# Optimization experiments

Hardware: AMD Instinct MI355X
Metric: run time of the kernel (lower is better)

The kernel has to match this reference:

```python
import jax, jax.numpy as jnp
import numpy as np

N_NODES = 10000
N_EDGES = 320000
IN_DIM = 256
HID = 64
HEADS = 4
OUT_DIM = 64
NEG_SLOPE = 0.2


def setup_inputs() -> dict:
    key = jax.random.key(0)
    ks = jax.random.split(key, 10)
    s = 0.05
    return {
        "h": jax.random.normal(ks[0], (N_NODES, IN_DIM), jnp.float32),
        "src": jax.random.randint(ks[1], (N_EDGES,), 0, N_NODES, jnp.int32),
        "dst": jax.random.randint(ks[2], (N_EDGES,), 0, N_NODES, jnp.int32),
        "W1": jax.random.normal(ks[3], (IN_DIM, HEADS * HID), jnp.float32) * s,
        "al1": jax.random.normal(ks[4], (HEADS, HID), jnp.float32) * s,
        "ar1": jax.random.normal(ks[5], (HEADS, HID), jnp.float32) * s,
        "b1": jnp.zeros((HEADS * HID,), jnp.float32),
        "W2": jax.random.normal(ks[6], (HEADS * HID, OUT_DIM), jnp.float32) * s,
        "al2": jax.random.normal(ks[7], (1, OUT_DIM), jnp.float32) * s,
        "ar2": jax.random.normal(ks[8], (1, OUT_DIM), jnp.float32) * s,
        "b2": jnp.zeros((OUT_DIM,), jnp.float32),
    }


def _gatconv(h, W, al, ar, b, src, dst, n_heads, d_out):
    """DGL-style GATConv: project, edge-softmax attention, scatter-aggregate."""
    n = h.shape[0]
    feat = (h @ W).reshape(n, n_heads, d_out)          # [N,H,D]
    el = jnp.sum(feat * al, axis=-1)                   # [N,H]
    er = jnp.sum(feat * ar, axis=-1)                   # [N,H]
    e = jax.nn.leaky_relu(el[src] + er[dst], NEG_SLOPE)  # [E,H]
    # segment softmax over incoming edges of each dst node
    m = jax.ops.segment_max(e, dst, num_segments=n)    # [N,H]
    ex = jnp.exp(e - m[dst])                           # [E,H]
    denom = jax.ops.segment_sum(ex, dst, num_segments=n)  # [N,H]
    alpha = ex / denom[dst]                            # [E,H]
    msg = feat[src] * alpha[:, :, None]                # [E,H,D]
    out = jax.ops.segment_sum(msg, dst, num_segments=n)  # [N,H,D]
    return out + b.reshape(n_heads, d_out)


def reference(h, src, dst, W1, al1, ar1, b1, W2, al2, ar2, b2):
    h1 = _gatconv(h, W1, al1, ar1, b1, src, dst, HEADS, HID)
    h1 = jax.nn.elu(h1.reshape(N_NODES, HEADS * HID))  # flatten(1) then ELU
    h2 = _gatconv(h1, W2, al2, ar2, b2, src, dst, 1, OUT_DIM)
    return jnp.squeeze(h2, axis=1)  # [N, OUT_DIM]
```

## Files before the change

kernel.cpp:

```cpp
#include <hip/hip_runtime.h>
#include <hip/hip_bf16.h>
#include <stdint.h>

#define NN 10000
#define NE 320000
#define NH 4
#define BCAP 128

#define GEMM1_MB 79
#define GEMM1_BLOCKS (GEMM1_MB * 4)
#define BUILD_BLOCKS 1250

typedef __attribute__((ext_vector_type(8))) short s16x8;
typedef __attribute__((ext_vector_type(4))) float f32x4;
typedef __attribute__((ext_vector_type(8))) unsigned short u16x8;

static __device__ __forceinline__ float b2f(unsigned short u) {
    union { unsigned int i; float f; } x; x.i = ((unsigned int)u) << 16; return x.f;
}
static __device__ __forceinline__ unsigned short f2b(float f) {
    unsigned int u = __float_as_uint(f);
    unsigned int r = (u + 0x7fffu + ((u >> 16) & 1u)) >> 16;
    return (unsigned short)r;
}

__global__ __launch_bounds__(256) void k_prep(const unsigned short* __restrict__ hraw,
                        const void* __restrict__ W1, const void* __restrict__ W2,
                        const void* al1, const void* ar1, const void* b1,
                        const void* al2, const void* ar2, const void* b2,
                        unsigned short* __restrict__ W1T, unsigned short* __restrict__ W2T,
                        unsigned short* __restrict__ canon, int* __restrict__ cnt,
                        int* __restrict__ flag) {
    __shared__ int sb[256];
    int t = threadIdx.x;
    int c = 0;
    for (int i = t; i < 2048; i += 256) {
        unsigned short u = hraw[i];
        int e = (u >> 7) & 0xFF;
        c += (e >= 97 && e <= 157) ? 1 : 0;
    }
    sb[t] = c;
    __syncthreads();
    for (int o = 128; o > 0; o >>= 1) {
        if (t < o) sb[t] += sb[t + o];
        __syncthreads();
    }
    int isbf = (sb[0] >= 1741) ? 1 : 0;

    int idx = blockIdx.x * 256 + t;
    if (idx < 65536) {
        int n = idx >> 8, k = idx & 255;
        W1T[idx] = isbf ? ((const unsigned short*)W1)[k * 256 + n]
                        : f2b(((const float*)W1)[k * 256 + n]);
    } else if (idx < 81920) {
        int j = idx - 65536;
        int n = j >> 8, k = j & 255;
        W2T[j] = isbf ? ((const unsigned short*)W2)[k * 64 + n]
                      : f2b(((const float*)W2)[k * 64 + n]);
    } else if (idx < 82880) {
        int j = idx - 81920;
        const void* srcp; int q;
        if      (j < 256) { srcp = al1; q = j; }
        else if (j < 512) { srcp = ar1; q = j - 256; }
        else if (j < 768) { srcp = b1;  q = j - 512; }
        else if (j < 832) { srcp = al2; q = j - 768; }
        else if (j < 896) { srcp = ar2; q = j - 832; }
        else              { srcp = b2;  q = j - 896; }
        canon[j] = isbf ? ((const unsigned short*)srcp)[q] : f2b(((const float*)srcp)[q]);
    } else if (idx < 92880) {
        cnt[idx - 82880] = 0;
    } else if (idx == 92880) {
        flag[0] = isbf;
    }
}

#define BSTRIDE 264
static __device__ __forceinline__ void gemm_body(short* Bs,
                        const void* __restrict__ A, const unsigned short* __restrict__ BT,
                        unsigned short* __restrict__ C,
                        float* __restrict__ el, float* __restrict__ er,
                        const unsigned short* __restrict__ al,
                        const unsigned short* __restrict__ ar,
                        int M, int N, int H, int a_isbf, int mtile, int head) {
    int t = threadIdx.x;
    int wave = t >> 6, lane = t & 63;
    int m0 = mtile * 128;
    const unsigned short* Bh = BT + (size_t)head * 64 * 256;

#pragma unroll
    for (int i = 0; i < 8; ++i) {
        int idx = t + i * 256;
        int row = idx >> 5, chunk = idx & 31;
        *(s16x8*)&Bs[row * BSTRIDE + chunk * 8] =
            *(const s16x8*)&Bh[(size_t)row * 256 + chunk * 8];
    }
    __syncthreads();

    int kq = (lane >> 4) * 8;
    const unsigned short* Ab = (const unsigned short*)A;
    const float*          Af = (const float*)A;
    int aR[2];
#pragma unroll
    for (int mi = 0; mi < 2; ++mi) {
        int aRow = m0 + mi * 64 + wave * 16 + (lane & 15);
        aR[mi] = (aRow < M) ? aRow : M - 1;
    }
    f32x4 acc[2][4] = {};

#pragma unroll
    for (int k0 = 0; k0 < 256; k0 += 32) {
        s16x8 afr[2];
#pragma unroll
        for (int mi = 0; mi < 2; ++mi) {
            if (a_isbf) {
                afr[mi] = *(const s16x8*)&Ab[(size_t)aR[mi] * 256 + k0 + kq];
            } else {
                const float* pf = &Af[(size_t)aR[mi] * 256 + k0 + kq];
                float4 x0 = *(const float4*)pf;
                float4 x1 = *(const float4*)(pf + 4);
                afr[mi][0] = (short)f2b(x0.x); afr[mi][1] = (short)f2b(x0.y);
                afr[mi][2] = (short)f2b(x0.z); afr[mi][3] = (short)f2b(x0.w);
                afr[mi][4] = (short)f2b(x1.x); afr[mi][5] = (short)f2b(x1.y);
                afr[mi][6] = (short)f2b(x1.z); afr[mi][7] = (short)f2b(x1.w);
            }
        }
#pragma unroll
        for (int nt = 0; nt < 4; ++nt) {
            s16x8 bfr = *(const s16x8*)&Bs[(nt * 16 + (lane & 15)) * BSTRIDE + k0 + kq];
            acc[0][nt] = __builtin_amdgcn_mfma_f32_16x16x32_bf16(afr[0], bfr, acc[0][nt], 0, 0, 0);
            acc[1][nt] = __builtin_amdgcn_mfma_f32_16x16x32_bf16(afr[1], bfr, acc[1][nt], 0, 0, 0);
        }
    }

    float alv[4], arv[4];
#pragma unroll
    for (int nt = 0; nt < 4; ++nt) {
        int c = (lane & 15) + nt * 16;
        alv[nt] = b2f(al[head * 64 + c]);
        arv[nt] = b2f(ar[head * 64 + c]);
    }
    int col0 = head * 64 + (lane & 15);
#pragma unroll
    for (int mi = 0; mi < 2; ++mi) {
        int r0 = m0 + mi * 64 + wave * 16 + (lane >> 4) * 4;
        float cr[4][4];
#pragma unroll
        for (int nt = 0; nt < 4; ++nt) {
            int col = col0 + nt * 16;
#pragma unroll
            for (int i = 0; i < 4; ++i) {
                unsigned short cb = f2b(acc[mi][nt][i]);
                cr[nt][i] = b2f(cb);
                int r = r0 + i;
                if (r < M) C[(size_t)r * N + col] = cb;
            }
        }
#pragma unroll
        for (int i = 0; i < 4; ++i) {
            float pl = 0.f, pr = 0.f;
#pragma unroll
            for (int nt = 0; nt < 4; ++nt) {
                pl += cr[nt][i] * alv[nt];
                pr += cr[nt][i] * arv[nt];
            }
#pragma unroll
            for (int o = 1; o < 16; o <<= 1) {
                pl += __shfl_xor(pl, o, 64);
                pr += __shfl_xor(pr, o, 64);
            }
            int r = r0 + i;
            if ((lane & 15) == 0 && r < M) {
                el[(size_t)r * H + head] = pl;
                er[(size_t)r * H + head] = pr;
            }
        }
    }
}

__global__ __launch_bounds__(256) void k_g1b(const void* __restrict__ A,
                        const unsigned short* __restrict__ W1T,
                        unsigned short* __restrict__ feat1,
                        float* __restrict__ el, float* __restrict__ er,
                        const unsigned short* __restrict__ al,
                        const unsigned short* __restrict__ ar,
                        const int* __restrict__ flagp,
                        const int* __restrict__ src, const int* __restrict__ dst,
                        int* __restrict__ cnt, int* __restrict__ bucket) {
    __shared__ short Bs[64 * BSTRIDE];
    int bid = blockIdx.x;
    if (bid < GEMM1_BLOCKS) {
        int head = bid / GEMM1_MB;
        int mtile = bid - head * GEMM1_MB;
        gemm_body(Bs, A, W1T, feat1, el, er, al, ar, NN, 256, NH, flagp[0], mtile, head);
    } else {
        int i = (bid - GEMM1_BLOCKS) * 256 + threadIdx.x;
        if (i < NE) {
            int d = dst[i];
            int pos = atomicAdd(&cnt[d], 1);
            if (pos < BCAP) bucket[(d << 7) + pos] = src[i];
        }
    }
}

__global__ __launch_bounds__(256) void k_gemm(const void* __restrict__ A,
                                              const unsigned short* __restrict__ BT,
                                              unsigned short* __restrict__ C,
                                              float* __restrict__ el, float* __restrict__ er,
                                              const unsigned short* __restrict__ al,
                                              const unsigned short* __restrict__ ar,
                                              int M, int N, int H) {
    __shared__ short Bs[64 * BSTRIDE];
    gemm_body(Bs, A, BT, C, el, er, al, ar, M, N, H, 1, blockIdx.x, blockIdx.y);
}

__global__ __launch_bounds__(256) void k_edge1(const int* __restrict__ cnt,
                        const int* __restrict__ bucket,
                        const float* __restrict__ el, const float* __restrict__ er,
                        const unsigned short* __restrict__ feat,
                        const unsigned short* __restrict__ b1,
                        unsigned short* __restrict__ h1) {
    int wave = threadIdx.x >> 6, lane = threadIdx.x & 63;
    int node = blockIdx.x * 4 + wave;
    if (node >= NN) return;
    int eg = lane >> 3, d8 = lane & 7;
    int end = cnt[node]; if (end > BCAP) end = BCAP;
    const int* bkt = bucket + ((size_t)node << 7);
    float4 er4 = *(const float4*)&er[(size_t)node * 4];

    if (end <= 64) {
        int s = 0;
        float w0 = 0.f, w1 = 0.f, w2 = 0.f, w3 = 0.f;
        if (lane < end) {
            s = bkt[lane];
            float4 el4 = *(const float4*)&el[(size_t)s * 4];
            float x0 = el4.x + er4.x; x0 = (x0 >= 0.f) ? x0 : 0.2f * x0;
            float x1 = el4.y + er4.y; x1 = (x1 >= 0.f) ? x1 : 0.2f * x1;
            float x2 = el4.z + er4.z; x2 = (x2 >= 0.f) ? x2 : 0.2f * x2;
            float x3 = el4.w + er4.w; x3 = (x3 >= 0.f) ? x3 : 0.2f * x3;
            w0 = __expf(x0); w1 = __expf(x1);
            w2 = __expf(x2); w3 = __expf(x3);
        }
        int niter = (end + 7) >> 3;
#pragma unroll
        for (int h = 0; h < 4; ++h) {
            float wh = (h == 0) ? w0 : (h == 1) ? w1 : (h == 2) ? w2 : w3;
            float a[8] = {};
            for (int i = 0; i < niter; ++i) {
                int idx = 8 * i + eg;
                float we = __shfl(wh, idx, 64);
                int   se = __shfl(s, idx, 64);
                u16x8 fv = *(const u16x8*)&feat[(((size_t)se * NH + h) << 6) + (d8 << 3)];
#pragma unroll
                for (int j = 0; j < 8; ++j) a[j] += we * b2f(fv[j]);
            }
            float ls = wh;
#pragma unroll
            for (int o = 1; o < 64; o <<= 1) ls += __shfl_xor(ls, o, 64);
#pragma unroll
            for (int j = 0; j < 8; ++j) {
                a[j] += __shfl_xor(a[j], 8, 64);
                a[j] += __shfl_xor(a[j], 16, 64);
                a[j] += __shfl_xor(a[j], 32, 64);
            }
            if (eg == 0) {
                float inv = (ls > 0.f) ? 1.f / ls : 0.f;
                u16x8 r;
#pragma unroll
                for (int j = 0; j < 8; ++j) {
                    float o = a[j] * inv + b2f(b1[h * 64 + d8 * 8 + j]);
                    o = (o > 0.f) ? o : (__expf(o) - 1.f);
                    r[j] = f2b(o);
                }
                *(u16x8*)&h1[(((size_t)node * NH + h) << 6) + d8 * 8] = r;
            }
        }
    } else {
        float a[4][8] = {};
        float ls0 = 0.f, ls1 = 0.f, ls2 = 0.f, ls3 = 0.f;
        for (int base = 0; base < end; base += 64) {
            int c = base + lane;
            int s = 0;
            float w0 = 0.f, w1 = 0.f, w2 = 0.f, w3 = 0.f;
            if (c < end) {
                s = bkt[c];
                float4 el4 = *(const float4*)&el[(size_t)s * 4];
                float x0 = el4.x + er4.x; x0 = (x0 >= 0.f) ? x0 : 0.2f * x0;
                float x1 = el4.y + er4.y; x1 = (x1 >= 0.f) ? x1 : 0.2f * x1;
                float x2 = el4.z + er4.z; x2 = (x2 >= 0.f) ? x2 : 0.2f * x2;
                float x3 = el4.w + er4.w; x3 = (x3 >= 0.f) ? x3 : 0.2f * x3;
                w0 = __expf(x0); w1 = __expf(x1);
                w2 = __expf(x2); w3 = __expf(x3);
            }
            ls0 += w0; ls1 += w1; ls2 += w2; ls3 += w3;
            int cn = end - base; if (cn > 64) cn = 64;
            int niter = (cn + 7) >> 3;
#pragma unroll
            for (int h = 0; h < 4; ++h) {
                float wh = (h == 0) ? w0 : (h == 1) ? w1 : (h == 2) ? w2 : w3;
                for (int i = 0; i < niter; ++i) {
                    int idx = 8 * i + eg;
                    float we = __shfl(wh, idx, 64);
                    int   se = __shfl(s, idx, 64);
                    u16x8 fv = *(const u16x8*)&feat[(((size_t)se * NH + h) << 6) + (d8 << 3)];
#pragma unroll
                    for (int j = 0; j < 8; ++j) a[h][j] += we * b2f(fv[j]);
                }
            }
        }
#pragma unroll
        for (int h = 0; h < 4; ++h) {
            float ls = (h == 0) ? ls0 : (h == 1) ? ls1 : (h == 2) ? ls2 : ls3;
#pragma unroll
            for (int o = 1; o < 64; o <<= 1) ls += __shfl_xor(ls, o, 64);
#pragma unroll
            for (int j = 0; j < 8; ++j) {
                a[h][j] += __shfl_xor(a[h][j], 8, 64);
                a[h][j] += __shfl_xor(a[h][j], 16, 64);
                a[h][j] += __shfl_xor(a[h][j], 32, 64);
            }
            if (eg == 0) {
                float inv = (ls > 0.f) ? 1.f / ls : 0.f;
                u16x8 r;
#pragma unroll
                for (int j = 0; j < 8; ++j) {
                    float o = a[h][j] * inv + b2f(b1[h * 64 + d8 * 8 + j]);
                    o = (o > 0.f) ? o : (__expf(o) - 1.f);
                    r[j] = f2b(o);
                }
                *(u16x8*)&h1[(((size_t)node * NH + h) << 6) + d8 * 8] = r;
            }
        }
    }
}

__global__ __launch_bounds__(256) void k_edge2(const int* __restrict__ cnt,
                        const int* __restrict__ bucket,
                        const float* __restrict__ el, const float* __restrict__ er,
                        const unsigned short* __restrict__ feat,
                        const unsigned short* __restrict__ b2,
                        void* __restrict__ out, const int* __restrict__ flagp) {
    int wave = threadIdx.x >> 6, lane = threadIdx.x & 63;
    int node = blockIdx.x * 4 + wave;
    if (node >= NN) return;
    int eg = lane >> 3, d8 = lane & 7;
    int isbf = flagp[0];
    int end = cnt[node]; if (end > BCAP) end = BCAP;
    const int* bkt = bucket + ((size_t)node << 7);
    float er_d = er[node];
    float lsum = 0.f;
    float a[8] = {};
    for (int base = 0; base < end; base += 64) {
        int c = base + lane;
        float wgt = 0.f; int s = 0;
        if (c < end) {
            s = bkt[c];
            float x = el[s] + er_d;
            x = (x >= 0.f) ? x : 0.2f * x;
            wgt = __expf(x);
        }
        lsum += wgt;
        int cn = end - base; if (cn > 64) cn = 64;
        int niter = (cn + 7) >> 3;
#pragma unroll 2
        for (int i = 0; i < niter; ++i) {
            int idx = 8 * i + eg;
            float we = __shfl(wgt, idx, 64);
            int   se = __shfl(s, idx, 64);
            u16x8 fv = *(const u16x8*)&feat[((size_t)se << 6) + (d8 << 3)];
#pragma unroll
            for (int j = 0; j < 8; ++j) a[j] += we * b2f(fv[j]);
        }
    }
#pragma unroll
    for (int o = 1; o < 64; o <<= 1) lsum += __shfl_xor(lsum, o, 64);
#pragma unroll
    for (int j = 0; j < 8; ++j) {
        a[j] += __shfl_xor(a[j], 8, 64);
        a[j] += __shfl_xor(a[j], 16, 64);
        a[j] += __shfl_xor(a[j], 32, 64);
    }
    if (eg == 0) {
        float inv = (lsum > 0.f) ? 1.f / lsum : 0.f;
        float o[8];
#pragma unroll
        for (int j = 0; j < 8; ++j) o[j] = a[j] * inv + b2f(b2[d8 * 8 + j]);
        size_t ob = ((size_t)node << 6) + d8 * 8;
        if (isbf) {
            u16x8 r;
#pragma unroll
            for (int j = 0; j < 8; ++j) r[j] = f2b(o[j]);
            *(u16x8*)&((unsigned short*)out)[ob] = r;
        } else {
            float4 r0, r1;
            r0.x = o[0]; r0.y = o[1]; r0.z = o[2]; r0.w = o[3];
            r1.x = o[4]; r1.y = o[5]; r1.z = o[6]; r1.w = o[7];
            *(float4*)&((float*)out)[ob] = r0;
            *(float4*)&((float*)out)[ob + 4] = r1;
        }
    }
}

extern "C" void kernel_launch(void* const* d_in, const int* in_sizes, int n_in,
                              void* d_out, int out_size, void* d_ws, size_t ws_size,
                              hipStream_t stream) {
    const void* h   = d_in[0];
    const int*  src = (const int*)d_in[1];
    const int*  dst = (const int*)d_in[2];
    const void* W1  = d_in[3];
    const void* al1 = d_in[4];
    const void* ar1 = d_in[5];
    const void* b1  = d_in[6];
    const void* W2  = d_in[7];
    const void* al2 = d_in[8];
    const void* ar2 = d_in[9];
    const void* b2  = d_in[10];

    char* w = (char*)d_ws;
    size_t off = 0;
    auto alloc = [&](size_t bytes) -> void* {
        void* p = w + off;
        off = (off + bytes + 255) & ~(size_t)255;
        return p;
    };
    int* flag               = (int*)alloc(8);
    int* cnt                = (int*)alloc(NN * 4);
    int* bucket             = (int*)alloc((size_t)NN * BCAP * 4);
    unsigned short* canon   = (unsigned short*)alloc(960 * 2);
    unsigned short* W1T     = (unsigned short*)alloc(256 * 256 * 2);
    unsigned short* W2T     = (unsigned short*)alloc(64 * 256 * 2);
    unsigned short* feat1   = (unsigned short*)alloc((size_t)NN * 256 * 2);
    float* el1              = (float*)alloc(NN * NH * 4);
    float* er1              = (float*)alloc(NN * NH * 4);
    unsigned short* h1      = (unsigned short*)alloc((size_t)NN * 256 * 2);
    unsigned short* feat2   = (unsigned short*)alloc((size_t)NN * 64 * 2);
    float* el2              = (float*)alloc(NN * 4);
    float* er2              = (float*)alloc(NN * 4);
    (void)ws_size; (void)in_sizes; (void)n_in; (void)out_size;

    unsigned short* cal1 = canon + 0;
    unsigned short* car1 = canon + 256;
    unsigned short* cb1  = canon + 512;
    unsigned short* cal2 = canon + 768;
    unsigned short* car2 = canon + 832;
    unsigned short* cb2  = canon + 896;

    k_prep<<<363, 256, 0, stream>>>((const unsigned short*)h, W1, W2,
                                    al1, ar1, b1, al2, ar2, b2,
                                    W1T, W2T, canon, cnt, flag);
    k_g1b<<<GEMM1_BLOCKS + BUILD_BLOCKS, 256, 0, stream>>>(h, W1T, feat1, el1, er1,
                                                           cal1, car1, flag,
                                                           src, dst, cnt, bucket);
    k_edge1<<<(NN + 3) / 4, 256, 0, stream>>>(cnt, bucket, el1, er1, feat1, cb1, h1);
    k_gemm<<<dim3(GEMM1_MB, 1), 256, 0, stream>>>(h1, W2T, feat2, el2, er2,
                                                  cal2, car2, NN, 64, 1);
    k_edge2<<<(NN + 3) / 4, 256, 0, stream>>>(cnt, bucket, el2, er2, feat2, cb2, d_out, flag);
}
```

Measured before the change: 157.9 us.

## Fuse all GAT stages into one persistent cooperative kernel with grid syncs

Replaces the five separate launches (prep, GEMM1+bucket build, edge1, GEMM2, edge2) with a single cooperative persistent kernel. Each block loops over the work units of every stage, and the stages are separated by grid-wide syncs. The aim is to remove per-launch overhead and the inter-kernel gaps. In exchange, occupancy is capped at 4 blocks per CU, and every block redundantly recomputes the bf16 input-detection reduction. The old multi-kernel path remains as a fallback if the cooperative launch fails.

```diff
diff --git a/kernel.cpp b/kernel.cpp
--- a/kernel.cpp
+++ b/kernel.cpp
@@ -1,6 +1,9 @@
 #include <hip/hip_runtime.h>
+#include <hip/hip_cooperative_groups.h>
 #include <hip/hip_bf16.h>
 #include <stdint.h>
+
+namespace cg = cooperative_groups;
 
 #define NN 10000
 #define NE 320000
@@ -10,6 +13,7 @@
 #define GEMM1_MB 79
 #define GEMM1_BLOCKS (GEMM1_MB * 4)
 #define BUILD_BLOCKS 1250
+#define PREP_UNITS 363
 
 typedef __attribute__((ext_vector_type(8))) short s16x8;
 typedef __attribute__((ext_vector_type(4))) float f32x4;
@@ -22,6 +26,388 @@
     unsigned int u = __float_as_uint(f);
     unsigned int r = (u + 0x7fffu + ((u >> 16) & 1u)) >> 16;
     return (unsigned short)r;
+}
+
+#define BSTRIDE 264
+static __device__ __forceinline__ void gemm_body(short* Bs,
+                        const void* __restrict__ A, const unsigned short* __restrict__ BT,
+                        unsigned short* __restrict__ C,
+                        float* __restrict__ el, float* __restrict__ er,
+                        const unsigned short* __restrict__ al,
+                        const unsigned short* __restrict__ ar,
+                        int M, int N, int H, int a_isbf, int mtile, int head) {
+    int t = threadIdx.x;
+    int wave = t >> 6, lane = t & 63;
+    int m0 = mtile * 128;
+    const unsigned short* Bh = BT + (size_t)head * 64 * 256;
+
+    __syncthreads();
+#pragma unroll
+    for (int i = 0; i < 8; ++i) {
+        int idx = t + i * 256;
+        int row = idx >> 5, chunk = idx & 31;
+        *(s16x8*)&Bs[row * BSTRIDE + chunk * 8] =
+            *(const s16x8*)&Bh[(size_t)row * 256 + chunk * 8];
+    }
+    __syncthreads();
+
+    int kq = (lane >> 4) * 8;
+    const unsigned short* Ab = (const unsigned short*)A;
+    const float*          Af = (const float*)A;
+    int aR[2];
+#pragma unroll
+    for (int mi = 0; mi < 2; ++mi) {
+        int aRow = m0 + mi * 64 + wave * 16 + (lane & 15);
+        aR[mi] = (aRow < M) ? aRow : M - 1;
+    }
+    f32x4 acc[2][4] = {};
+
+#pragma unroll
+    for (int k0 = 0; k0 < 256; k0 += 32) {
+        s16x8 afr[2];
+#pragma unroll
+        for (int mi = 0; mi < 2; ++mi) {
+            if (a_isbf) {
+                afr[mi] = *(const s16x8*)&Ab[(size_t)aR[mi] * 256 + k0 + kq];
+            } else {
+                const float* pf = &Af[(size_t)aR[mi] * 256 + k0 + kq];
+                float4 x0 = *(const float4*)pf;
+                float4 x1 = *(const float4*)(pf + 4);
+                afr[mi][0] = (short)f2b(x0.x); afr[mi][1] = (short)f2b(x0.y);
+                afr[mi][2] = (short)f2b(x0.z); afr[mi][3] = (short)f2b(x0.w);
+                afr[mi][4] = (short)f2b(x1.x); afr[mi][5] = (short)f2b(x1.y);
+                afr[mi][6] = (short)f2b(x1.z); afr[mi][7] = (short)f2b(x1.w);
+            }
+        }
+#pragma unroll
+        for (int nt = 0; nt < 4; ++nt) {
+            s16x8 bfr = *(const s16x8*)&Bs[(nt * 16 + (lane & 15)) * BSTRIDE + k0 + kq];
+            acc[0][nt] = __builtin_amdgcn_mfma_f32_16x16x32_bf16(afr[0], bfr, acc[0][nt], 0, 0, 0);
+            acc[1][nt] = __builtin_amdgcn_mfma_f32_16x16x32_bf16(afr[1], bfr, acc[1][nt], 0, 0, 0);
+        }
+    }
+
+    float alv[4], arv[4];
+#pragma unroll
+    for (int nt = 0; nt < 4; ++nt) {
+        int c = (lane & 15) + nt * 16;
+        alv[nt] = b2f(al[head * 64 + c]);
+        arv[nt] = b2f(ar[head * 64 + c]);
+    }
+    int col0 = head * 64 + (lane & 15);
+#pragma unroll
+    for (int mi = 0; mi < 2; ++mi) {
+        int r0 = m0 + mi * 64 + wave * 16 + (lane >> 4) * 4;
+        float cr[4][4];
+#pragma unroll
+        for (int nt = 0; nt < 4; ++nt) {
+            int col = col0 + nt * 16;
+#pragma unroll
+            for (int i = 0; i < 4; ++i) {
+                unsigned short cb = f2b(acc[mi][nt][i]);
+                cr[nt][i] = b2f(cb);
+                int r = r0 + i;
+                if (r < M) C[(size_t)r * N + col] = cb;
+            }
+        }
+#pragma unroll
+        for (int i = 0; i < 4; ++i) {
+            float pl = 0.f, pr = 0.f;
+#pragma unroll
+            for (int nt = 0; nt < 4; ++nt) {
+                pl += cr[nt][i] * alv[nt];
+                pr += cr[nt][i] * arv[nt];
+            }
+#pragma unroll
+            for (int o = 1; o < 16; o <<= 1) {
+                pl += __shfl_xor(pl, o, 64);
+                pr += __shfl_xor(pr, o, 64);
+            }
+            int r = r0 + i;
+            if ((lane & 15) == 0 && r < M) {
+                el[(size_t)r * H + head] = pl;
+                er[(size_t)r * H + head] = pr;
+            }
+        }
+    }
+}
+
+static __device__ __forceinline__ void edge1_unit(int node,
+                        const int* __restrict__ cnt, const int* __restrict__ bucket,
+                        const float* __restrict__ el, const float* __restrict__ er,
+                        const unsigned short* __restrict__ feat,
+                        const unsigned short* __restrict__ b1,
+                        unsigned short* __restrict__ h1, int lane) {
+    int eg = lane >> 3, d8 = lane & 7;
+    int end = cnt[node]; if (end > BCAP) end = BCAP;
+    const int* bkt = bucket + ((size_t)node << 7);
+    float4 er4 = *(const float4*)&er[(size_t)node * 4];
+
+    if (end <= 64) {
+        int s = 0;
+        float w0 = 0.f, w1 = 0.f, w2 = 0.f, w3 = 0.f;
+        if (lane < end) {
+            s = bkt[lane];
+            float4 el4 = *(const float4*)&el[(size_t)s * 4];
+            float x0 = el4.x + er4.x; x0 = (x0 >= 0.f) ? x0 : 0.2f * x0;
+            float x1 = el4.y + er4.y; x1 = (x1 >= 0.f) ? x1 : 0.2f * x1;
+            float x2 = el4.z + er4.z; x2 = (x2 >= 0.f) ? x2 : 0.2f * x2;
+            float x3 = el4.w + er4.w; x3 = (x3 >= 0.f) ? x3 : 0.2f * x3;
+            w0 = __expf(x0); w1 = __expf(x1);
+            w2 = __expf(x2); w3 = __expf(x3);
+        }
+        int niter = (end + 7) >> 3;
+#pragma unroll
+        for (int h = 0; h < 4; ++h) {
+            float wh = (h == 0) ? w0 : (h == 1) ? w1 : (h == 2) ? w2 : w3;
+            float a[8] = {};
+            for (int i = 0; i < niter; ++i) {
+                int idx = 8 * i + eg;
+                float we = __shfl(wh, idx, 64);
+                int   se = __shfl(s, idx, 64);
+                u16x8 fv = *(const u16x8*)&feat[(((size_t)se * NH + h) << 6) + (d8 << 3)];
+#pragma unroll
+                for (int j = 0; j < 8; ++j) a[j] += we * b2f(fv[j]);
+            }
+            float ls = wh;
+#pragma unroll
+            for (int o = 1; o < 64; o <<= 1) ls += __shfl_xor(ls, o, 64);
+#pragma unroll
+            for (int j = 0; j < 8; ++j) {
+                a[j] += __shfl_xor(a[j], 8, 64);
+                a[j] += __shfl_xor(a[j], 16, 64);
+                a[j] += __shfl_xor(a[j], 32, 64);
+            }
+            if (eg == 0) {
+                float inv = (ls > 0.f) ? 1.f / ls : 0.f;
+                u16x8 r;
+#pragma unroll
+                for (int j = 0; j < 8; ++j) {
+                    float o = a[j] * inv + b2f(b1[h * 64 + d8 * 8 + j]);
+                    o = (o > 0.f) ? o : (__expf(o) - 1.f);
+                    r[j] = f2b(o);
+                }
+                *(u16x8*)&h1[(((size_t)node * NH + h) << 6) + d8 * 8] = r;
+            }
+        }
+    } else {
+        float a[4][8] = {};
+        float ls0 = 0.f, ls1 = 0.f, ls2 = 0.f, ls3 = 0.f;
+        for (int base = 0; base < end; base += 64) {
+            int c = base + lane;
+            int s = 0;
+            float w0 = 0.f, w1 = 0.f, w2 = 0.f, w3 = 0.f;
+            if (c < end) {
+                s = bkt[c];
+                float4 el4 = *(const float4*)&el[(size_t)s * 4];
+                float x0 = el4.x + er4.x; x0 = (x0 >= 0.f) ? x0 : 0.2f * x0;
+                float x1 = el4.y + er4.y; x1 = (x1 >= 0.f) ? x1 : 0.2f * x1;
+                float x2 = el4.z + er4.z; x2 = (x2 >= 0.f) ? x2 : 0.2f * x2;
+                float x3 = el4.w + er4.w; x3 = (x3 >= 0.f) ? x3 : 0.2f * x3;
+                w0 = __expf(x0); w1 = __expf(x1);
+                w2 = __expf(x2); w3 = __expf(x3);
+            }
+            ls0 += w0; ls1 += w1; ls2 += w2; ls3 += w3;
+            int cn = end - base; if (cn > 64) cn = 64;
+            int niter = (cn + 7) >> 3;
+#pragma unroll
+            for (int h = 0; h < 4; ++h) {
+                float wh = (h == 0) ? w0 : (h == 1) ? w1 : (h == 2) ? w2 : w3;
+                for (int i = 0; i < niter; ++i) {
+                    int idx = 8 * i + eg;
+                    float we = __shfl(wh, idx, 64);
+                    int   se = __shfl(s, idx, 64);
+                    u16x8 fv = *(const u16x8*)&feat[(((size_t)se * NH + h) << 6) + (d8 << 3)];
+#pragma unroll
+                    for (int j = 0; j < 8; ++j) a[h][j] += we * b2f(fv[j]);
+                }
+            }
+        }
+#pragma unroll
+        for (int h = 0; h < 4; ++h) {
+            float ls = (h == 0) ? ls0 : (h == 1) ? ls1 : (h == 2) ? ls2 : ls3;
+#pragma unroll
+            for (int o = 1; o < 64; o <<= 1) ls += __shfl_xor(ls, o, 64);
+#pragma unroll
+            for (int j = 0; j < 8; ++j) {
+                a[h][j] += __shfl_xor(a[h][j], 8, 64);
+                a[h][j] += __shfl_xor(a[h][j], 16, 64);
+                a[h][j] += __shfl_xor(a[h][j], 32, 64);
+            }
+            if (eg == 0) {
+                float inv = (ls > 0.f) ? 1.f / ls : 0.f;
+                u16x8 r;
+#pragma unroll
+                for (int j = 0; j < 8; ++j) {
+                    float o = a[h][j] * inv + b2f(b1[h * 64 + d8 * 8 + j]);
+                    o = (o > 0.f) ? o : (__expf(o) - 1.f);
+                    r[j] = f2b(o);
+                }
+                *(u16x8*)&h1[(((size_t)node * NH + h) << 6) + d8 * 8] = r;
+            }
+        }
+    }
+}
+
+static __device__ __forceinline__ void edge2_unit(int node,
+                        const int* __restrict__ cnt, const int* __restrict__ bucket,
+                        const float* __restrict__ el, const float* __restrict__ er,
+                        const unsigned short* __restrict__ feat,
+                        const unsigned short* __restrict__ b2,
+                        void* __restrict__ out, int isbf, int lane) {
+    int eg = lane >> 3, d8 = lane & 7;
+    int end = cnt[node]; if (end > BCAP) end = BCAP;
+    const int* bkt = bucket + ((size_t)node << 7);
+    float er_d = er[node];
+    float lsum = 0.f;
+    float a[8] = {};
+    for (int base = 0; base < end; base += 64) {
+        int c = base + lane;
+        float wgt = 0.f; int s = 0;
+        if (c < end) {
+            s = bkt[c];
+            float x = el[s] + er_d;
+            x = (x >= 0.f) ? x : 0.2f * x;
+            wgt = __expf(x);
+        }
+        lsum += wgt;
+        int cn = end - base; if (cn > 64) cn = 64;
+        int niter = (cn + 7) >> 3;
+#pragma unroll 2
+        for (int i = 0; i < niter; ++i) {
+            int idx = 8 * i + eg;
+            float we = __shfl(wgt, idx, 64);
+            int   se = __shfl(s, idx, 64);
+            u16x8 fv = *(const u16x8*)&feat[((size_t)se << 6) + (d8 << 3)];
+#pragma unroll
+            for (int j = 0; j < 8; ++j) a[j] += we * b2f(fv[j]);
+        }
+    }
+#pragma unroll
+    for (int o = 1; o < 64; o <<= 1) lsum += __shfl_xor(lsum, o, 64);
+#pragma unroll
+    for (int j = 0; j < 8; ++j) {
+        a[j] += __shfl_xor(a[j], 8, 64);
+        a[j] += __shfl_xor(a[j], 16, 64);
+        a[j] += __shfl_xor(a[j], 32, 64);
+    }
+    if (eg == 0) {
+        float inv = (lsum > 0.f) ? 1.f / lsum : 0.f;
+        float o[8];
+#pragma unroll
+        for (int j = 0; j < 8; ++j) o[j] = a[j] * inv + b2f(b2[d8 * 8 + j]);
+        size_t ob = ((size_t)node << 6) + d8 * 8;
+        if (isbf) {
+            u16x8 r;
+#pragma unroll
+            for (int j = 0; j < 8; ++j) r[j] = f2b(o[j]);
+            *(u16x8*)&((unsigned short*)out)[ob] = r;
+        } else {
+            float4 r0, r1;
+            r0.x = o[0]; r0.y = o[1]; r0.z = o[2]; r0.w = o[3];
+            r1.x = o[4]; r1.y = o[5]; r1.z = o[6]; r1.w = o[7];
+            *(float4*)&((float*)out)[ob] = r0;
+            *(float4*)&((float*)out)[ob + 4] = r1;
+        }
+    }
+}
+
+__global__ __launch_bounds__(256, 4) void k_fused(
+        const void* __restrict__ h, const int* __restrict__ src, const int* __restrict__ dst,
+        const void* __restrict__ W1, const void* __restrict__ al1, const void* __restrict__ ar1,
+        const void* __restrict__ b1, const void* __restrict__ W2, const void* __restrict__ al2,
+        const void* __restrict__ ar2, const void* __restrict__ b2,
+        unsigned short* __restrict__ W1T, unsigned short* __restrict__ W2T,
+        unsigned short* __restrict__ canon, int* __restrict__ cnt, int* __restrict__ bucket,
+        unsigned short* __restrict__ feat1, float* __restrict__ el1, float* __restrict__ er1,
+        unsigned short* __restrict__ h1, unsigned short* __restrict__ feat2,
+        float* __restrict__ el2, float* __restrict__ er2, void* __restrict__ outp) {
+    __shared__ short Bs[64 * BSTRIDE];
+    __shared__ int sb[256];
+    cg::grid_group gg = cg::this_grid();
+    int t = threadIdx.x;
+    int wave = t >> 6, lane = t & 63;
+    int nb = gridDim.x;
+
+    {
+        int c = 0;
+        const unsigned short* hraw = (const unsigned short*)h;
+        for (int i = t; i < 2048; i += 256) {
+            unsigned short u = hraw[i];
+            int e = (u >> 7) & 0xFF;
+            c += (e >= 97 && e <= 157) ? 1 : 0;
+        }
+        sb[t] = c;
+        __syncthreads();
+        for (int o = 128; o > 0; o >>= 1) {
+            if (t < o) sb[t] += sb[t + o];
+            __syncthreads();
+        }
+    }
+    int isbf = (sb[0] >= 1741) ? 1 : 0;
+
+    for (int u = blockIdx.x; u < PREP_UNITS; u += nb) {
+        int idx = u * 256 + t;
+        if (idx < 65536) {
+            int n = idx >> 8, k = idx & 255;
+            W1T[idx] = isbf ? ((const unsigned short*)W1)[k * 256 + n]
+                            : f2b(((const float*)W1)[k * 256 + n]);
+        } else if (idx < 81920) {
+            int j = idx - 65536;
+            int n = j >> 8, k = j & 255;
+            W2T[j] = isbf ? ((const unsigned short*)W2)[k * 64 + n]
+                          : f2b(((const float*)W2)[k * 64 + n]);
+        } else if (idx < 82880) {
+            int j = idx - 81920;
+            const void* srcp; int q;
+            if      (j < 256) { srcp = al1; q = j; }
+            else if (j < 512) { srcp = ar1; q = j - 256; }
+            else if (j < 768) { srcp = b1;  q = j - 512; }
+            else if (j < 832) { srcp = al2; q = j - 768; }
+            else if (j < 896) { srcp = ar2; q = j - 832; }
+            else              { srcp = b2;  q = j - 896; }
+            canon[j] = isbf ? ((const unsigned short*)srcp)[q] : f2b(((const float*)srcp)[q]);
+        } else if (idx < 92880) {
+            cnt[idx - 82880] = 0;
+        }
+    }
+    gg.sync();
+
+    for (int u = blockIdx.x; u < GEMM1_BLOCKS + BUILD_BLOCKS; u += nb) {
+        if (u < GEMM1_BLOCKS) {
+            int head = u / GEMM1_MB;
+            int mtile = u - head * GEMM1_MB;
+            gemm_body(Bs, h, W1T, feat1, el1, er1, canon + 0, canon + 256,
+                      NN, 256, NH, isbf, mtile, head);
+        } else {
+            int i = (u - GEMM1_BLOCKS) * 256 + t;
+            if (i < NE) {
+                int d = dst[i];
+                int pos = atomicAdd(&cnt[d], 1);
+                if (pos < BCAP) bucket[(d << 7) + pos] = src[i];
+            }
+        }
+    }
+    gg.sync();
+
+    for (int u = blockIdx.x; u < (NN + 3) / 4; u += nb) {
+        int node = u * 4 + wave;
+        if (node < NN)
+            edge1_unit(node, cnt, bucket, el1, er1, feat1, canon + 512, h1, lane);
+    }
+    gg.sync();
+
+    for (int u = blockIdx.x; u < GEMM1_MB; u += nb) {
+        gemm_body(Bs, h1, W2T, feat2, el2, er2, canon + 768, canon + 832,
+                  NN, 64, 1, 1, u, 0);
+    }
+    gg.sync();
+
+    for (int u = blockIdx.x; u < (NN + 3) / 4; u += nb) {
+        int node = u * 4 + wave;
+        if (node < NN)
+            edge2_unit(node, cnt, bucket, el2, er2, feat2, canon + 896, outp, isbf, lane);
+    }
 }
 
 __global__ __launch_bounds__(256) void k_prep(const unsigned short* __restrict__ hraw,
@@ -74,109 +460,6 @@
     }
 }
 
-#define BSTRIDE 264
-static __device__ __forceinline__ void gemm_body(short* Bs,
-                        const void* __restrict__ A, const unsigned short* __restrict__ BT,
-                        unsigned short* __restrict__ C,
-                        float* __restrict__ el, float* __restrict__ er,
-                        const unsigned short* __restrict__ al,
-                        const unsigned short* __restrict__ ar,
-                        int M, int N, int H, int a_isbf, int mtile, int head) {
-    int t = threadIdx.x;
-    int wave = t >> 6, lane = t & 63;
-    int m0 = mtile * 128;
-    const unsigned short* Bh = BT + (size_t)head * 64 * 256;
-
-#pragma unroll
-    for (int i = 0; i < 8; ++i) {
-        int idx = t + i * 256;
-        int row = idx >> 5, chunk = idx & 31;
-        *(s16x8*)&Bs[row * BSTRIDE + chunk * 8] =
-            *(const s16x8*)&Bh[(size_t)row * 256 + chunk * 8];
-    }
-    __syncthreads();
-
-    int kq = (lane >> 4) * 8;
-    const unsigned short* Ab = (const unsigned short*)A;
-    const float*          Af = (const float*)A;
-    int aR[2];
-#pragma unroll
-    for (int mi = 0; mi < 2; ++mi) {
-        int aRow = m0 + mi * 64 + wave * 16 + (lane & 15);
-        aR[mi] = (aRow < M) ? aRow : M - 1;
-    }
-    f32x4 acc[2][4] = {};
-
-#pragma unroll
-    for (int k0 = 0; k0 < 256; k0 += 32) {
-        s16x8 afr[2];
-#pragma unroll
-        for (int mi = 0; mi < 2; ++mi) {
-            if (a_isbf) {
-                afr[mi] = *(const s16x8*)&Ab[(size_t)aR[mi] * 256 + k0 + kq];
-            } else {
-                const float* pf = &Af[(size_t)aR[mi] * 256 + k0 + kq];
-                float4 x0 = *(const float4*)pf;
-                float4 x1 = *(const float4*)(pf + 4);
-                afr[mi][0] = (short)f2b(x0.x); afr[mi][1] = (short)f2b(x0.y);
-                afr[mi][2] = (short)f2b(x0.z); afr[mi][3] = (short)f2b(x0.w);
-                afr[mi][4] = (short)f2b(x1.x); afr[mi][5] = (short)f2b(x1.y);
-                afr[mi][6] = (short)f2b(x1.z); afr[mi][7] = (short)f2b(x1.w);
-            }
-        }
-#pragma unroll
-        for (int nt = 0; nt < 4; ++nt) {
-            s16x8 bfr = *(const s16x8*)&Bs[(nt * 16 + (lane & 15)) * BSTRIDE + k0 + kq];
-            acc[0][nt] = __builtin_amdgcn_mfma_f32_16x16x32_bf16(afr[0], bfr, acc[0][nt], 0, 0, 0);
-            acc[1][nt] = __builtin_amdgcn_mfma_f32_16x16x32_bf16(afr[1], bfr, acc[1][nt], 0, 0, 0);
-        }
-    }
-
-    float alv[4], arv[4];
-#pragma unroll
-    for (int nt = 0; nt < 4; ++nt) {
-        int c = (lane & 15) + nt * 16;
-        alv[nt] = b2f(al[head * 64 + c]);
-        arv[nt] = b2f(ar[head * 64 + c]);
-    }
-    int col0 = head * 64 + (lane & 15);
-#pragma unroll
-    for (int mi = 0; mi < 2; ++mi) {
-        int r0 = m0 + mi * 64 + wave * 16 + (lane >> 4) * 4;
-        float cr[4][4];
-#pragma unroll
-        for (int nt = 0; nt < 4; ++nt) {
-            int col = col0 + nt * 16;
-#pragma unroll
-            for (int i = 0; i < 4; ++i) {
-                unsigned short cb = f2b(acc[mi][nt][i]);
-                cr[nt][i] = b2f(cb);
-                int r = r0 + i;
-                if (r < M) C[(size_t)r * N + col] = cb;
-            }
-        }
-#pragma unroll
-        for (int i = 0; i < 4; ++i) {
-            float pl = 0.f, pr = 0.f;
-#pragma unroll
-            for (int nt = 0; nt < 4; ++nt) {
-                pl += cr[nt][i] * alv[nt];
-                pr += cr[nt][i] * arv[nt];
-            }
-#pragma unroll
-            for (int o = 1; o < 16; o <<= 1) {
-                pl += __shfl_xor(pl, o, 64);
-                pr += __shfl_xor(pr, o, 64);
-            }
-            int r = r0 + i;
-            if ((lane & 15) == 0 && r < M) {
-                el[(size_t)r * H + head] = pl;
-                er[(size_t)r * H + head] = pr;
-            }
-        }
-    }
-}
-
 __global__ __launch_bounds__(256) void k_g1b(const void* __restrict__ A,
                         const unsigned short* __restrict__ W1T,
                         unsigned short* __restrict__ feat1,
@@ -222,115 +505,7 @@
     int wave = threadIdx.x >> 6, lane = threadIdx.x & 63;
     int node = blockIdx.x * 4 + wave;
     if (node >= NN) return;
-    int eg = lane >> 3, d8 = lane & 7;
-    int end = cnt[node]; if (end > BCAP) end = BCAP;
-    const int* bkt = bucket + ((size_t)node << 7);
-    float4 er4 = *(const float4*)&er[(size_t)node * 4];
-
-    if (end <= 64) {
-        int s = 0;
-        float w0 = 0.f, w1 = 0.f, w2 = 0.f, w3 = 0.f;
-        if (lane < end) {
-            s = bkt[lane];
-            float4 el4 = *(const float4*)&el[(size_t)s * 4];
-            float x0 = el4.x + er4.x; x0 = (x0 >= 0.f) ? x0 : 0.2f * x0;
-            float x1 = el4.y + er4.y; x1 = (x1 >= 0.f) ? x1 : 0.2f * x1;
-            float x2 = el4.z + er4.z; x2 = (x2 >= 0.f) ? x2 : 0.2f * x2;
-            float x3 = el4.w + er4.w; x3 = (x3 >= 0.f) ? x3 : 0.2f * x3;
-            w0 = __expf(x0); w1 = __expf(x1);
-            w2 = __expf(x2); w3 = __expf(x3);
-        }
-        int niter = (end + 7) >> 3;
-#pragma unroll
-        for (int h = 0; h < 4; ++h) {
-            float wh = (h == 0) ? w0 : (h == 1) ? w1 : (h == 2) ? w2 : w3;
-            float a[8] = {};
-            for (int i = 0; i < niter; ++i) {
-                int idx = 8 * i + eg;
-                float we = __shfl(wh, idx, 64);
-                int   se = __shfl(s, idx, 64);
-                u16x8 fv = *(const u16x8*)&feat[(((size_t)se * NH + h) << 6) + (d8 << 3)];
-#pragma unroll
-                for (int j = 0; j < 8; ++j) a[j] += we * b2f(fv[j]);
-            }
-            float ls = wh;
-#pragma unroll
-            for (int o = 1; o < 64; o <<= 1) ls += __shfl_xor(ls, o, 64);
-#pragma unroll
-            for (int j = 0; j < 8; ++j) {
-                a[j] += __shfl_xor(a[j], 8, 64);
-                a[j] += __shfl_xor(a[j], 16, 64);
-                a[j] += __shfl_xor(a[j], 32, 64);
-            }
-            if (eg == 0) {
-                float inv = (ls > 0.f) ? 1.f / ls : 0.f;
-                u16x8 r;
-#pragma unroll
-                for (int j = 0; j < 8; ++j) {
-                    float o = a[j] * inv + b2f(b1[h * 64 + d8 * 8 + j]);
-                    o = (o > 0.f) ? o : (__expf(o) - 1.f);
-                    r[j] = f2b(o);
-                }
-                *(u16x8*)&h1[(((size_t)node * NH + h) << 6) + d8 * 8] = r;
-            }
-        }
-    } else {
-        float a[4][8] = {};
-        float ls0 = 0.f, ls1 = 0.f, ls2 = 0.f, ls3 = 0.f;
-        for (int base = 0; base < end; base += 64) {
-            int c = base + lane;
-            int s = 0;
-            float w0 = 0.f, w1 = 0.f, w2 = 0.f, w3 = 0.f;
-            if (c < end) {
-                s = bkt[c];
-                float4 el4 = *(const float4*)&el[(size_t)s * 4];
-                float x0 = el4.x + er4.x; x0 = (x0 >= 0.f) ? x0 : 0.2f * x0;
-                float x1 = el4.y + er4.y; x1 = (x1 >= 0.f) ? x1 : 0.2f * x1;
-                float x2 = el4.z + er4.z; x2 = (x2 >= 0.f) ? x2 : 0.2f * x2;
-                float x3 = el4.w + er4.w; x3 = (x3 >= 0.f) ? x3 : 0.2f * x3;
-                w0 = __expf(x0); w1 = __expf(x1);
-                w2 = __expf(x2); w3 = __expf(x3);
-            }
-            ls0 += w0; ls1 += w1; ls2 += w2; ls3 += w3;
-            int cn = end - base; if (cn > 64) cn = 64;
-            int niter = (cn + 7) >> 3;
-#pragma unroll
-            for (int h = 0; h < 4; ++h) {
-                float wh = (h == 0) ? w0 : (h == 1) ? w1 : (h == 2) ? w2 : w3;
-                for (int i = 0; i < niter; ++i) {
-                    int idx = 8 * i + eg;
-                    float we = __shfl(wh, idx, 64);
-                    int   se = __shfl(s, idx, 64);
-                    u16x8 fv = *(const u16x8*)&feat[(((size_t)se * NH + h) << 6) + (d8 << 3)];
-#pragma unroll
-                    for (int j = 0; j < 8; ++j) a[h][j] += we * b2f(fv[j]);
-                }
-            }
-        }
-#pragma unroll
-        for (int h = 0; h < 4; ++h) {
-            float ls = (h == 0) ? ls0 : (h == 1) ? ls1 : (h == 2) ? ls2 : ls3;
-#pragma unroll
-            for (int o = 1; o < 64; o <<= 1) ls += __shfl_xor(ls, o, 64);
-#pragma unroll
-            for (int j = 0; j < 8; ++j) {
-                a[h][j] += __shfl_xor(a[h][j], 8, 64);
-                a[h][j] += __shfl_xor(a[h][j], 16, 64);
-                a[h][j] += __shfl_xor(a[h][j], 32, 64);
-            }
-            if (eg == 0) {
-                float inv = (ls > 0.f) ? 1.f / ls : 0.f;
-                u16x8 r;
-#pragma unroll
-                for (int j = 0; j < 8; ++j) {
-                    float o = a[h][j] * inv + b2f(b1[h * 64 + d8 * 8 + j]);
-                    o = (o > 0.f) ? o : (__expf(o) - 1.f);
-                    r[j] = f2b(o);
-                }
-                *(u16x8*)&h1[(((size_t)node * NH + h) << 6) + d8 * 8] = r;
-            }
-        }
-    }
+    edge1_unit(node, cnt, bucket, el, er, feat, b1, h1, lane);
 }
 
 __global__ __launch_bounds__(256) void k_edge2(const int* __restrict__ cnt,
@@ -342,62 +517,7 @@
     int wave = threadIdx.x >> 6, lane = threadIdx.x & 63;
     int node = blockIdx.x * 4 + wave;
     if (node >= NN) return;
-    int eg = lane >> 3, d8 = lane & 7;
-    int isbf = flagp[0];
-    int end = cnt[node]; if (end > BCAP) end = BCAP;
-    const int* bkt = bucket + ((size_t)node << 7);
-    float er_d = er[node];
-    float lsum = 0.f;
-    float a[8] = {};
-    for (int base = 0; base < end; base += 64) {
-        int c = base + lane;
-        float wgt = 0.f; int s = 0;
-        if (c < end) {
-            s = bkt[c];
-            float x = el[s] + er_d;
-            x = (x >= 0.f) ? x : 0.2f * x;
-            wgt = __expf(x);
-        }
-        lsum += wgt;
-        int cn = end - base; if (cn > 64) cn = 64;
-        int niter = (cn + 7) >> 3;
-#pragma unroll 2
-        for (int i = 0; i < niter; ++i) {
-            int idx = 8 * i + eg;
-            float we = __shfl(wgt, idx, 64);
-            int   se = __shfl(s, idx, 64);
-            u16x8 fv = *(const u16x8*)&feat[((size_t)se << 6) + (d8 << 3)];
-#pragma unroll
-            for (int j = 0; j < 8; ++j) a[j] += we * b2f(fv[j]);
-        }
-    }
-#pragma unroll
-    for (int o = 1; o < 64; o <<= 1) lsum += __shfl_xor(lsum, o, 64);
-#pragma unroll
-    for (int j = 0; j < 8; ++j) {
-        a[j] += __shfl_xor(a[j], 8, 64);
-        a[j] += __shfl_xor(a[j], 16, 64);
-        a[j] += __shfl_xor(a[j], 32, 64);
-    }
-    if (eg == 0) {
-        float inv = (lsum > 0.f) ? 1.f / lsum : 0.f;
-        float o[8];
-#pragma unroll
-        for (int j = 0; j < 8; ++j) o[j] = a[j] * inv + b2f(b2[d8 * 8 + j]);
-        size_t ob = ((size_t)node << 6) + d8 * 8;
-        if (isbf) {
-            u16x8 r;
-#pragma unroll
-            for (int j = 0; j < 8; ++j) r[j] = f2b(o[j]);
-            *(u16x8*)&((unsigned short*)out)[ob] = r;
-        } else {
-            float4 r0, r1;
-            r0.x = o[0]; r0.y = o[1]; r0.z = o[2]; r0.w = o[3];
-            r1.x = o[4]; r1.y = o[5]; r1.z = o[6]; r1.w = o[7];
-            *(float4*)&((float*)out)[ob] = r0;
-            *(float4*)&((float*)out)[ob + 4] = r1;
-        }
-    }
+    edge2_unit(node, cnt, bucket, el, er, feat, b2, out, flagp[0], lane);
 }
 
 extern "C" void kernel_launch(void* const* d_in, const int* in_sizes, int n_in,
@@ -443,6 +563,23 @@
     unsigned short* cal2 = canon + 768;
     unsigned short* car2 = canon + 832;
     unsigned short* cb2  = canon + 896;
+    void* outp = d_out;
+
+    int maxb = 0;
+    hipError_t oe = hipOccupancyMaxActiveBlocksPerMultiprocessor(
+        &maxb, reinterpret_cast<const void*>(k_fused), 256, 0);
+    if (oe != hipSuccess || maxb < 1) maxb = 1;
+    if (maxb > 4) maxb = 4;
+    int gridn = maxb * 256;
+
+    void* args[] = { (void*)&h, (void*)&src, (void*)&dst, (void*)&W1, (void*)&al1,
+                     (void*)&ar1, (void*)&b1, (void*)&W2, (void*)&al2, (void*)&ar2,
+                     (void*)&b2, (void*)&W1T, (void*)&W2T, (void*)&canon, (void*)&cnt,
+                     (void*)&bucket, (void*)&feat1, (void*)&el1, (void*)&er1, (void*)&h1,
+                     (void*)&feat2, (void*)&el2, (void*)&er2, (void*)&outp };
+    hipError_t le = hipLaunchCooperativeKernel(reinterpret_cast<const void*>(k_fused),
+                                               dim3(gridn), dim3(256), args, 0, stream);
+    if (le == hipSuccess) return;
 
     k_prep<<<363, 256, 0, stream>>>((const unsigned short*)h, W1, W2,
                                     al1, ar1, b1, al2, ar2, b2,
```

Result: slower. 409.8 us (+159.6%).

## Fuse layer-1 edge aggregation with layer-2 projection GEMM via shared memory

Applied to the files above, without the earlier changes.

Merges the layer-1 edge softmax/aggregation kernel with the layer-2 GEMM and attention-logit computation into one kernel. Each 512-thread block aggregates 16 nodes into shared memory and then runs a small MFMA GEMM against W2T to produce feat2, el2 and er2 directly. This removes the h1 round trip through global memory and one kernel launch. In exchange, the block must wait at syncthreads for every wave's aggregation to finish, W2T is reloaded from global memory in every block, and only 4 of the 8 waves run the GEMM phase.

```diff
diff --git a/kernel.cpp b/kernel.cpp
--- a/kernel.cpp
+++ b/kernel.cpp
@@ -202,26 +202,12 @@
     }
 }
 
-__global__ __launch_bounds__(256) void k_gemm(const void* __restrict__ A,
-                                              const unsigned short* __restrict__ BT,
-                                              unsigned short* __restrict__ C,
-                                              float* __restrict__ el, float* __restrict__ er,
-                                              const unsigned short* __restrict__ al,
-                                              const unsigned short* __restrict__ ar,
-                                              int M, int N, int H) {
-    __shared__ short Bs[64 * BSTRIDE];
-    gemm_body(Bs, A, BT, C, el, er, al, ar, M, N, H, 1, blockIdx.x, blockIdx.y);
-}
-
-__global__ __launch_bounds__(256) void k_edge1(const int* __restrict__ cnt,
-                        const int* __restrict__ bucket,
+static __device__ __forceinline__ void edge1_unit(int node,
+                        const int* __restrict__ cnt, const int* __restrict__ bucket,
                         const float* __restrict__ el, const float* __restrict__ er,
                         const unsigned short* __restrict__ feat,
                         const unsigned short* __restrict__ b1,
-                        unsigned short* __restrict__ h1) {
-    int wave = threadIdx.x >> 6, lane = threadIdx.x & 63;
-    int node = blockIdx.x * 4 + wave;
-    if (node >= NN) return;
+                        unsigned short* __restrict__ h1row, int lane) {
     int eg = lane >> 3, d8 = lane & 7;
     int end = cnt[node]; if (end > BCAP) end = BCAP;
     const int* bkt = bucket + ((size_t)node << 7);
@@ -271,7 +257,7 @@
                     o = (o > 0.f) ? o : (__expf(o) - 1.f);
                     r[j] = f2b(o);
                 }
-                *(u16x8*)&h1[(((size_t)node * NH + h) << 6) + d8 * 8] = r;
+                *(u16x8*)&h1row[h * 64 + d8 * 8] = r;
             }
         }
     } else {
@@ -327,7 +313,88 @@
                     o = (o > 0.f) ? o : (__expf(o) - 1.f);
                     r[j] = f2b(o);
                 }
-                *(u16x8*)&h1[(((size_t)node * NH + h) << 6) + d8 * 8] = r;
+                *(u16x8*)&h1row[h * 64 + d8 * 8] = r;
+            }
+        }
+    }
+}
+
+#define H1S 264
+__global__ __launch_bounds__(512, 4) void k_e1g2(const int* __restrict__ cnt,
+                        const int* __restrict__ bucket,
+                        const float* __restrict__ el, const float* __restrict__ er,
+                        const unsigned short* __restrict__ feat,
+                        const unsigned short* __restrict__ b1,
+                        const unsigned short* __restrict__ W2T,
+                        const unsigned short* __restrict__ al2,
+                        const unsigned short* __restrict__ ar2,
+                        unsigned short* __restrict__ feat2,
+                        float* __restrict__ el2, float* __restrict__ er2) {
+    __shared__ unsigned short h1s[16 * H1S];
+    __shared__ unsigned short f2s[16 * 72];
+    int t = threadIdx.x;
+    int wave = t >> 6, lane = t & 63;
+    int nb0 = blockIdx.x * 16;
+
+#pragma unroll
+    for (int r = 0; r < 2; ++r) {
+        int lrow = wave * 2 + r;
+        edge1_unit(nb0 + lrow, cnt, bucket, el, er, feat, b1, &h1s[lrow * H1S], lane);
+    }
+    __syncthreads();
+
+    if (wave < 4) {
+        int m = lane & 15;
+        int kq = (lane >> 4) * 8;
+        int colB = wave * 16 + m;
+        const unsigned short* wp = &W2T[(size_t)colB * 256];
+        f32x4 acc = {};
+#pragma unroll
+        for (int k0 = 0; k0 < 256; k0 += 32) {
+            s16x8 af = *(const s16x8*)&h1s[m * H1S + k0 + kq];
+            s16x8 bf = *(const s16x8*)&wp[k0 + kq];
+            acc = __builtin_amdgcn_mfma_f32_16x16x32_bf16(af, bf, acc, 0, 0, 0);
+        }
+        int r0 = (lane >> 4) * 4;
+#pragma unroll
+        for (int i = 0; i < 4; ++i) {
+            unsigned short cb = f2b(acc[i]);
+            int row = r0 + i;
+            feat2[(size_t)(nb0 + row) * 64 + colB] = cb;
+            f2s[row * 72 + colB] = cb;
+        }
+    }
+    __syncthreads();
+
+    if (wave == 0) {
+        int c = lane & 15;
+        float alv[4], arv[4];
+#pragma unroll
+        for (int nt = 0; nt < 4; ++nt) {
+            alv[nt] = b2f(al2[c + nt * 16]);
+            arv[nt] = b2f(ar2[c + nt * 16]);
+        }
+        int r0 = (lane >> 4) * 4;
+#pragma unroll
+        for (int i = 0; i < 4; ++i) {
+            int row = r0 + i;
+            float cr[4];
+#pragma unroll
+            for (int nt = 0; nt < 4; ++nt) cr[nt] = b2f(f2s[row * 72 + c + nt * 16]);
+            float pl = 0.f, pr = 0.f;
+#pragma unroll
+            for (int nt = 0; nt < 4; ++nt) {
+                pl += cr[nt] * alv[nt];
+                pr += cr[nt] * arv[nt];
+            }
+#pragma unroll
+            for (int o = 1; o < 16; o <<= 1) {
+                pl += __shfl_xor(pl, o, 64);
+                pr += __shfl_xor(pr, o, 64);
+            }
+            if ((lane & 15) == 0) {
+                el2[nb0 + row] = pl;
+                er2[nb0 + row] = pr;
             }
         }
     }
@@ -431,7 +498,6 @@
     unsigned short* feat1   = (unsigned short*)alloc((size_t)NN * 256 * 2);
     float* el1              = (float*)alloc(NN * NH * 4);
     float* er1              = (float*)alloc(NN * NH * 4);
-    unsigned short* h1      = (unsigned short*)alloc((size_t)NN * 256 * 2);
     unsigned short* feat2   = (unsigned short*)alloc((size_t)NN * 64 * 2);
     float* el2              = (float*)alloc(NN * 4);
     float* er2              = (float*)alloc(NN * 4);
@@ -450,8 +516,7 @@
     k_g1b<<<GEMM1_BLOCKS + BUILD_BLOCKS, 256, 0, stream>>>(h, W1T, feat1, el1, er1,
                                                            cal1, car1, flag,
                                                            src, dst, cnt, bucket);
-    k_edge1<<<(NN + 3) / 4, 256, 0, stream>>>(cnt, bucket, el1, er1, feat1, cb1, h1);
-    k_gemm<<<dim3(GEMM1_MB, 1), 256, 0, stream>>>(h1, W2T, feat2, el2, er2,
-                                                  cal2, car2, NN, 64, 1);
+    k_e1g2<<<NN / 16, 512, 0, stream>>>(cnt, bucket, el1, er1, feat1, cb1,
+                                        W2T, cal2, car2, feat2, el2, er2);
     k_edge2<<<(NN + 3) / 4, 256, 0, stream>>>(cnt, bucket, el2, er2, feat2, cb2, d_out, flag);
 }
```

Result: no change. 159.1 us (+0.8%).
